# Performance work log

Measured on AMD Instinct MI355X. Metric: run time of the kernel, lower is better.

Reference implementation:

```python
import jax, jax.numpy as jnp
import numpy as np

B, N, DIM = 2, 512, 512
HEADS, DIM_HEAD, MAX_LEN = 8, 64, 1024


def _skew(QEr):
    # pad last dim on the left by 1, reshape (n, n+1) -> (n+1, n), drop first row
    padded = jnp.pad(QEr, ((0, 0), (0, 0), (0, 0), (1, 0)))
    b, h, r, c = padded.shape
    return padded.reshape(b, h, c, r)[:, :, 1:, :]


def _fft_multiply_parallel(A, x):
    # A: [b,h,n,n] decay matrix; x: [b,h,n,d]
    b, h, n, d = x.shape
    # y = [last column of A, first row of A] -> [b,h,2n]
    y = jnp.concatenate([A[:, :, :, -1], A[:, :, 0, :]], axis=-1)
    v = jnp.concatenate([x, jnp.zeros_like(x)], axis=-2)  # zero-pad rows n -> 2n
    # Faithful to the original torch code: fftn over ALL axes (incl. batch/head),
    # then ifft over the LAST axis only, then slice back to n rows.
    H = jnp.fft.fftn(y)[:, :, :, None] * jnp.fft.fftn(v)
    return jnp.fft.ifft(H)[:, :, :n, :]


def _forward(x, Wq, Wk, Wv, Er):
    b, n, _ = x.shape

    def split_heads(t):
        return t.reshape(b, n, HEADS, DIM_HEAD).transpose(0, 2, 1, 3)  # [b,h,n,d]

    q = split_heads(x @ Wq)
    k = split_heads(x @ Wk)
    v = split_heads(x @ Wv)
    # global (Frobenius) norm over the full tensor, as torch.norm(t)
    q = q / jnp.linalg.norm(q)
    k = k / jnp.linalg.norm(k)
    q_ = jax.nn.elu(q)
    k_ = jax.nn.elu(k)

    Er_t = Er[MAX_LEN - n:, :].T        # [d, n]
    QEr = q @ Er_t                       # [b,h,n,n]
    c = jnp.exp(_skew(QEr))              # relative-position decay, [b,h,n,n]

    a_1 = jnp.einsum('bhnx,bhny->bhnxy', k_, v).reshape(b, HEADS, n, DIM_HEAD * DIM_HEAD)
    d_2 = _fft_multiply_parallel(c, k_)                                   # [b,h,n,d] complex
    d_1 = _fft_multiply_parallel(c, a_1).reshape(b, HEADS, n, DIM_HEAD, DIM_HEAD)

    top = jnp.einsum('bhnx,bhnyz->bhnz', q_, d_1)    # complex [b,h,n,d]
    bottom = jnp.einsum('bhnx,bhny->bhny', q_, d_2)  # complex [b,h,n,d]
    return top / bottom


def setup_inputs() -> dict:
    key = jax.random.key(0)
    k1, k2, k3, k4, k5 = jax.random.split(key, 5)
    s = jnp.float32(1.0 / np.sqrt(DIM))
    return {
        'x': jax.random.normal(k1, (B, N, DIM), dtype=jnp.float32),
        'Wq': jax.random.normal(k2, (DIM, HEADS * DIM_HEAD), dtype=jnp.float32) * s,
        'Wk': jax.random.normal(k3, (DIM, HEADS * DIM_HEAD), dtype=jnp.float32) * s,
        'Wv': jax.random.normal(k4, (DIM, HEADS * DIM_HEAD), dtype=jnp.float32) * s,
        'Er': jax.random.normal(k5, (MAX_LEN, DIM_HEAD), dtype=jnp.float32),
    }


def reference(x, Wq, Wk, Wv, Er):
    return _forward(x, Wq, Wk, Wv, Er)
```

## Files before the change

### kernel.cpp

```cpp
#include <hip/hip_runtime.h>
#include <math.h>


#define DIMX 512
#define NPOS 512
#define PADIDX(m) ((m) + ((m) >> 4))

typedef unsigned short ushort_t;
typedef unsigned int uint_t;
typedef __bf16 bf16x8 __attribute__((ext_vector_type(8)));
typedef float floatx4 __attribute__((ext_vector_type(4)));

static __device__ inline ushort_t f2bf(float f) {
    uint_t u = __float_as_uint(f);
    u = u + 0x7FFFu + ((u >> 16) & 1u);
    return (ushort_t)(u >> 16);
}
static __device__ inline float bf2f(ushort_t h) {
    return __uint_as_float(((uint_t)h) << 16);
}

__global__ __launch_bounds__(256)
void conv_kernel(const float* __restrict__ x,
                 const float* __restrict__ Wk, const float* __restrict__ Wv,
                 ushort_t* __restrict__ xh, ushort_t* __restrict__ xl,
                 ushort_t* __restrict__ wth, ushort_t* __restrict__ wtl)
{
    const int blk = blockIdx.x;
    const int t = threadIdx.x;
    if (blk < 512) {
        const int idx4 = blk * 256 + t;
        const float4 v = ((const float4*)x)[idx4];
        const float vf[4] = {v.x, v.y, v.z, v.w};
        ushort_t h[4], l[4];
        #pragma unroll
        for (int e = 0; e < 4; ++e) {
            h[e] = f2bf(vf[e]);
            l[e] = f2bf(vf[e] - bf2f(h[e]));
        }
        ushort_t* ph = xh + (size_t)idx4 * 4;
        ushort_t* pl = xl + (size_t)idx4 * 4;
        #pragma unroll
        for (int e = 0; e < 4; ++e) { ph[e] = h[e]; pl[e] = l[e]; }
    } else {
        __shared__ float tile[32][33];
        const int b2 = blk - 512;
        const int s  = b2 >> 8;
        const int kt = (b2 >> 4) & 15;
        const int nt = b2 & 15;
        const int c  = t & 31, r4 = t >> 5;
        const float* __restrict__ W = s ? Wv : Wk;
        #pragma unroll
        for (int i = 0; i < 4; ++i) {
            const int row = r4 + i * 8;
            tile[row][c] = W[(size_t)(kt * 32 + row) * 512 + nt * 32 + c];
        }
        __syncthreads();
        #pragma unroll
        for (int i = 0; i < 4; ++i) {
            const int nl = r4 + i * 8;
            const float v = tile[c][nl];
            const ushort_t h = f2bf(v);
            const ushort_t l = f2bf(v - bf2f(h));
            const size_t o = (size_t)(s * 512 + nt * 32 + nl) * 512 + kt * 32 + c;
            wth[o] = h;
            wtl[o] = l;
        }
    }
}

__global__ __launch_bounds__(256)
void gemm_mfma_kernel(const ushort_t* __restrict__ xh, const ushort_t* __restrict__ xl,
                      const ushort_t* __restrict__ wth, const ushort_t* __restrict__ wtl,
                      float* __restrict__ K, float* __restrict__ V,
                      float* __restrict__ partials)
{
    const int blk = blockIdx.x;
    const int ct = blk >> 5;
    const int rt = blk & 31;
    const int t = threadIdx.x;
    const int w = t >> 6, lane = t & 63;
    const int qd = lane >> 4, lm = lane & 15;
    const int mrow  = rt * 32 + (w >> 1) * 16 + lm;
    const int ncol0 = ct * 64 + (w & 1) * 32;
    const size_t aoff  = (size_t)mrow * 512 + qd * 8;
    const size_t boff0 = (size_t)(ncol0 + lm) * 512 + qd * 8;
    const size_t boff1 = (size_t)(ncol0 + 16 + lm) * 512 + qd * 8;

    floatx4 acc0 = {0.f, 0.f, 0.f, 0.f};
    floatx4 acc1 = {0.f, 0.f, 0.f, 0.f};

    #pragma unroll
    for (int ks = 0; ks < 16; ++ks) {
        const int k0 = ks * 32;
        const bf16x8 Ah  = *(const bf16x8*)&xh [aoff  + k0];
        const bf16x8 Al  = *(const bf16x8*)&xl [aoff  + k0];
        const bf16x8 B0h = *(const bf16x8*)&wth[boff0 + k0];
        const bf16x8 B0l = *(const bf16x8*)&wtl[boff0 + k0];
        const bf16x8 B1h = *(const bf16x8*)&wth[boff1 + k0];
        const bf16x8 B1l = *(const bf16x8*)&wtl[boff1 + k0];
        acc0 = __builtin_amdgcn_mfma_f32_16x16x32_bf16(Ah, B0h, acc0, 0, 0, 0);
        acc0 = __builtin_amdgcn_mfma_f32_16x16x32_bf16(Ah, B0l, acc0, 0, 0, 0);
        acc0 = __builtin_amdgcn_mfma_f32_16x16x32_bf16(Al, B0h, acc0, 0, 0, 0);
        acc1 = __builtin_amdgcn_mfma_f32_16x16x32_bf16(Ah, B1h, acc1, 0, 0, 0);
        acc1 = __builtin_amdgcn_mfma_f32_16x16x32_bf16(Ah, B1l, acc1, 0, 0, 0);
        acc1 = __builtin_amdgcn_mfma_f32_16x16x32_bf16(Al, B1h, acc1, 0, 0, 0);
    }

    __shared__ float red[4];
    float ss = 0.f;
    const int orow0 = rt * 32 + (w >> 1) * 16 + qd * 4;
    float* __restrict__ O = (ct < 8) ? K : V;
    const int cb = (ct < 8) ? 0 : 512;
    const int c0 = ncol0 + lm - cb;
    #pragma unroll
    for (int r = 0; r < 4; ++r) {
        const size_t row = orow0 + r;
        const float v0 = acc0[r], v1 = acc1[r];
        O[row * 512 + c0]      = v0;
        O[row * 512 + c0 + 16] = v1;
        if (ct < 8) ss += v0 * v0 + v1 * v1;
    }
    #pragma unroll
    for (int off = 32; off > 0; off >>= 1)
        ss += __shfl_down(ss, off, 64);
    if (lane == 0) red[w] = ss;
    __syncthreads();
    if (t == 0) partials[blk] = red[0] + red[1] + red[2] + red[3];
}

__device__ __constant__ float C8[8] = {
    1.f, 0.70710678118654752440f, 0.f, -0.70710678118654752440f,
   -1.f, -0.70710678118654752440f, 0.f, 0.70710678118654752440f };
__device__ __constant__ float S8[8] = {
    0.f, -0.70710678118654752440f, -1.f, -0.70710678118654752440f,
    0.f,  0.70710678118654752440f,  1.f,  0.70710678118654752440f };

__global__ __launch_bounds__(256)
void stage1_kernel(const float* __restrict__ K,
                   const float* __restrict__ V,
                   const float* __restrict__ partials,
                   float2* __restrict__ Gk,
                   float2* __restrict__ Gp)
{
    const int m = blockIdx.x;
    const int t = threadIdx.x;
    __shared__ float kk[2][8][64];
    __shared__ float pp[2][8][64];
    __shared__ float skp[16][4];
    __shared__ float sk[2][8];
    __shared__ float sred[4];

    float p = partials[t] + partials[t + 256];
    #pragma unroll
    for (int off = 32; off > 0; off >>= 1)
        p += __shfl_down(p, off, 64);
    if ((t & 63) == 0) sred[t >> 6] = p;
    __syncthreads();
    const float scale = (float)(1.0 / sqrt((double)sred[0] + (double)sred[1] +
                                           (double)sred[2] + (double)sred[3]));

    {
        const int e0 = t * 4;
        const int b = e0 >> 9, rem = e0 & 511, h = rem >> 6, z = rem & 63;
        const size_t src = (size_t)(b * 512 + m) * DIMX + h * 64 + z;
        const float4 kv4 = *(const float4*)&K[src];
        const float4 vv4 = *(const float4*)&V[src];
        const float kf[4] = {kv4.x, kv4.y, kv4.z, kv4.w};
        const float vf[4] = {vv4.x, vv4.y, vv4.z, vv4.w};
        #pragma unroll
        for (int e = 0; e < 4; ++e) {
            const float kv = kf[e] * scale;
            kk[b][h][z + e] = kv > 0.f ? kv : expm1f(kv);
            pp[b][h][z + e] = vf[e];
        }
    }
    __syncthreads();
    if (t < 64) {
        const int bh = t >> 2, q = t & 3;
        float s = 0.f;
        #pragma unroll
        for (int zz = 0; zz < 16; ++zz) s += kk[bh >> 3][bh & 7][q * 16 + zz];
        skp[bh][q] = s;
    }
    __syncthreads();
    if (t < 16) sk[t >> 3][t & 7] = skp[t][0] + skp[t][1] + skp[t][2] + skp[t][3];
    __syncthreads();
    for (int e = t; e < 1024; e += 256) {
        const int b = e >> 9, rem = e & 511, h = rem >> 6, z = rem & 63;
        pp[b][h][z] *= sk[b][h];
    }
    __syncthreads();

    for (int e2 = t; e2 < 512; e2 += 256) {
        const int be = e2 >> 5;
        const int zp = e2 & 31;
        const int beta = be >> 3, eta = be & 7;
        float4 rk, rp;
        #pragma unroll
        for (int zz = 0; zz < 2; ++zz) {
            const int z = zp * 2 + zz;
            float gkr = 0.f, gki = 0.f, gpr = 0.f, gpi = 0.f;
            #pragma unroll
            for (int b = 0; b < 2; ++b) {
                const float sgn = (beta & b) ? -1.f : 1.f;
                #pragma unroll
                for (int h = 0; h < 8; ++h) {
                    const int ph = (eta * h) & 7;
                    const float cr = C8[ph], ci = S8[ph];
                    const float a = kk[b][h][z] * sgn;
                    gkr = fmaf(a, cr, gkr); gki = fmaf(a, ci, gki);
                    const float p2 = pp[b][h][z] * sgn;
                    gpr = fmaf(p2, cr, gpr); gpi = fmaf(p2, ci, gpi);
                }
            }
            if (zz == 0) { rk.x = gkr; rk.y = gki; rp.x = gpr; rp.y = gpi; }
            else         { rk.z = gkr; rk.w = gki; rp.z = gpr; rp.w = gpi; }
        }
        const size_t o = ((size_t)be * NPOS + m) * 64 + zp * 2;
        *(float4*)&Gk[o] = rk;
        *(float4*)&Gp[o] = rp;
    }
}

__global__ __launch_bounds__(256)
void fft_div_kernel(const float2* __restrict__ Gk,
                    const float2* __restrict__ Gp,
                    float* __restrict__ out, int out_cplx)
{
    const int blk = blockIdx.x;
    const int j  = blk & 7;
    const int l  = (blk >> 3) & 3;
    const int be = blk >> 5;
    const int zg = j * 4 + l;
    const int t  = threadIdx.x;

    __shared__ float2 g[4][1088];
    __shared__ float2 w[544];

    for (int jj = t; jj < 512; jj += 256) {
        double s, cc;
        sincos(-6.2831853071795864769 * (double)jj / 1024.0, &s, &cc);
        w[PADIDX(jj)] = make_float2((float)cc, (float)s);
    }
    __syncthreads();

    for (int e = t; e < 1024; e += 256) {
        const int a = e >> 9;
        const int m = e & 511;
        const float4 v4 = *(const float4*)&(a ? Gp : Gk)[((size_t)be * NPOS + m) * 64 + zg * 2];
        const float2 v0 = make_float2(v4.x, v4.y);
        const float2 v1 = make_float2(v4.z, v4.w);
        const float2 tw = w[PADIDX(m)];
        g[a * 2 + 0][PADIDX(m)] = v0;
        g[a * 2 + 1][PADIDX(m)] = v1;
        g[a * 2 + 0][PADIDX(m + 512)] = make_float2(v0.x * tw.x - v0.y * tw.y,
                                                    v0.x * tw.y + v0.y * tw.x);
        g[a * 2 + 1][PADIDX(m + 512)] = make_float2(v1.x * tw.x - v1.y * tw.y,
                                                    v1.x * tw.y + v1.y * tw.x);
    }
    __syncthreads();

    #pragma unroll
    for (int s = 1; s <= 9; ++s) {
        const int S = 512 >> s;
        const int lg = 9 - s;
        #pragma unroll
        for (int q = 0; q < 8; ++q) {
            const int B    = t + 256 * q;
            const int arr  = B >> 9;
            const int beta = B & 511;
            const int jb   = beta & (S - 1);
            const int seg  = beta >> lg;
            const int u    = (seg << (lg + 1)) + jb;
            const int v    = u + S;
            const float2 tw = w[PADIDX(jb << s)];
            const float2 A  = g[arr][PADIDX(u)];
            const float2 Bb = g[arr][PADIDX(v)];
            g[arr][PADIDX(u)] = make_float2(A.x + Bb.x, A.y + Bb.y);
            const float sr = A.x - Bb.x, si = A.y - Bb.y;
            g[arr][PADIDX(v)] = make_float2(sr * tw.x - si * tw.y,
                                            sr * tw.y + si * tw.x);
        }
        __syncthreads();
    }

    for (int e2 = t; e2 < 512; e2 += 256) {
        const int i  = e2;
        const int pi = PADIDX(2 * i);
        const int mu = (int)(__brev((unsigned)i) >> 23);
        float4 res;
        #pragma unroll
        for (int zi = 0; zi < 2; ++zi) {
            const float2 D  = g[zi][pi];
            const float2 Nm = g[2 + zi][pi];
            const float inv = 1.f / (D.x * D.x + D.y * D.y);
            const float rr = (Nm.x * D.x + Nm.y * D.y) * inv;
            const float ri = (Nm.y * D.x - Nm.x * D.y) * inv;
            if (zi == 0) { res.x = rr; res.y = ri; }
            else         { res.z = rr; res.w = ri; }
        }
        const size_t o = ((size_t)be * NPOS + mu) * 64 + zg * 2;
        if (out_cplx) {
            *(float4*)&((float2*)out)[o] = res;
        } else {
            out[o]     = res.x;
            out[o + 1] = res.z;
        }
    }
}

__global__ __launch_bounds__(256)
void gemm_kv_kernel(const float* __restrict__ x,
                    const float* __restrict__ Wk,
                    const float* __restrict__ Wv,
                    float* __restrict__ K,
                    float* __restrict__ V,
                    float* __restrict__ partials)
{
    const int blk  = blockIdx.x;
    const int sel  = (blk >> 2) & 1;
    const int cg2  = blk & 3;
    const int rt   = blk >> 3;
    const int row0 = rt * 16;
    const int col0 = cg2 * 128;
    const int t    = threadIdx.x;
    const int tc   = t & 31;
    const int tr   = t >> 5;
    const float* __restrict__ W   = sel ? Wv : Wk;
    float* __restrict__       Out = sel ? V  : K;

    __shared__ float xs[16][DIMX];
    __shared__ float red[4];

    #pragma unroll
    for (int j = 0; j < 8; ++j) {
        const int f = t + j * 256;
        const int row = f >> 7, c4 = f & 127;
        *(float4*)&xs[row][c4 * 4] = *(const float4*)&x[(size_t)(row0 + row) * DIMX + c4 * 4];
    }
    __syncthreads();

    const float* Wb = W + col0 + tc * 4;
    float4 wA[8], wB[8];
    #pragma unroll
    for (int j = 0; j < 8; ++j) wA[j] = *(const float4*)&Wb[(size_t)(j) * DIMX];
    #pragma unroll
    for (int j = 0; j < 8; ++j) wB[j] = *(const float4*)&Wb[(size_t)(8 + j) * DIMX];

    float acc[2][4] = {{0,0,0,0},{0,0,0,0}};
    const int r0 = tr * 2;

    #define COMPUTE_CHUNK(WREG, CH)                                            \
        {   float4 xv0a = *(const float4*)&xs[r0][(CH) * 8];                   \
            float4 xv0b = *(const float4*)&xs[r0][(CH) * 8 + 4];               \
            float4 xv1a = *(const float4*)&xs[r0 + 1][(CH) * 8];               \
            float4 xv1b = *(const float4*)&xs[r0 + 1][(CH) * 8 + 4];           \
            _Pragma("unroll")                                                  \
            for (int kk = 0; kk < 4; ++kk) {                                   \
                const float x0 = (&xv0a.x)[kk], x1 = (&xv1a.x)[kk];            \
                _Pragma("unroll")                                              \
                for (int cc = 0; cc < 4; ++cc) {                               \
                    acc[0][cc] = fmaf(x0, (&WREG[kk].x)[cc], acc[0][cc]);      \
                    acc[1][cc] = fmaf(x1, (&WREG[kk].x)[cc], acc[1][cc]);      \
                } }                                                            \
            _Pragma("unroll")                                                  \
            for (int kk = 0; kk < 4; ++kk) {                                   \
                const float x0 = (&xv0b.x)[kk], x1 = (&xv1b.x)[kk];            \
                _Pragma("unroll")                                              \
                for (int cc = 0; cc < 4; ++cc) {                               \
                    acc[0][cc] = fmaf(x0, (&WREG[kk + 4].x)[cc], acc[0][cc]);  \
                    acc[1][cc] = fmaf(x1, (&WREG[kk + 4].x)[cc], acc[1][cc]);  \
                } } }

    for (int ch = 0; ch < 64; ch += 2) {
        COMPUTE_CHUNK(wA, ch)
        if (ch < 62) {
            #pragma unroll
            for (int j = 0; j < 8; ++j)
                wA[j] = *(const float4*)&Wb[(size_t)((ch + 2) * 8 + j) * DIMX];
        }
        COMPUTE_CHUNK(wB, ch + 1)
        if (ch < 62) {
            #pragma unroll
            for (int j = 0; j < 8; ++j)
                wB[j] = *(const float4*)&Wb[(size_t)((ch + 3) * 8 + j) * DIMX];
        }
    }
    #undef COMPUTE_CHUNK

    float ss = 0.f;
    #pragma unroll
    for (int i = 0; i < 2; ++i) {
        const int row = row0 + r0 + i;
        const float4 o = make_float4(acc[i][0], acc[i][1], acc[i][2], acc[i][3]);
        *(float4*)&Out[(size_t)row * DIMX + col0 + tc * 4] = o;
        ss += o.x * o.x + o.y * o.y + o.z * o.z + o.w * o.w;
    }
    if (sel == 0) {
        #pragma unroll
        for (int off = 32; off > 0; off >>= 1)
            ss += __shfl_down(ss, off, 64);
        if ((t & 63) == 0) red[t >> 6] = ss;
        __syncthreads();
        if (t == 0) partials[blk] = red[0] + red[1] + red[2] + red[3];
    } else {
        if (t == 0) partials[blk] = 0.f;
    }
}

__global__ __launch_bounds__(256)
void mdft_fallback_kernel(const float2* __restrict__ Gk,
                          const float2* __restrict__ Gp,
                          float* __restrict__ out,
                          int out_cplx)
{
    const int blk = blockIdx.x;
    const int be = blk >> 6, z = blk & 63;
    const int t = threadIdx.x;
    __shared__ float2 gk[512];
    __shared__ float2 gp[512];
    __shared__ float2 w[1024];

    for (int m = t; m < 512; m += 256) {
        const size_t idx = ((size_t)be * NPOS + m) * 64 + z;
        gk[m] = Gk[idx];
        gp[m] = Gp[idx];
    }
    for (int jj = t; jj < 1024; jj += 256) {
        double s, c;
        sincos(-6.2831853071795864769 * (double)jj / 1024.0, &s, &c);
        w[jj] = make_float2((float)c, (float)s);
    }
    __syncthreads();

    #pragma unroll
    for (int half = 0; half < 2; ++half) {
        const int mu = t + half * 256;
        double dr = 0.0, di = 0.0, nr = 0.0, ni = 0.0;
        int idx = 0;
        for (int m = 0; m < 512; ++m) {
            const float2 tw = w[idx];
            idx = (idx + mu) & 1023;
            const float2 a = gk[m];
            dr += (double)(a.x * tw.x - a.y * tw.y);
            di += (double)(a.x * tw.y + a.y * tw.x);
            const float2 p = gp[m];
            nr += (double)(p.x * tw.x - p.y * tw.y);
            ni += (double)(p.x * tw.y + p.y * tw.x);
        }
        const double dmag = dr * dr + di * di;
        const double orr = (nr * dr + ni * di) / dmag;
        const double oii = (ni * dr - nr * di) / dmag;
        const size_t o = ((size_t)be * NPOS + mu) * 64 + z;
        if (out_cplx) {
            out[2 * o]     = (float)orr;
            out[2 * o + 1] = (float)oii;
        } else {
            out[o] = (float)orr;
        }
    }
}

extern "C" void kernel_launch(void* const* d_in, const int* in_sizes, int n_in,
                              void* d_out, int out_size, void* d_ws, size_t ws_size,
                              hipStream_t stream)
{
    const float* x  = (const float*)d_in[0];
    const float* Wk = (const float*)d_in[2];
    const float* Wv = (const float*)d_in[3];
    float* out = (float*)d_out;

    char* ws = (char*)d_ws;
    float*  K    = (float*)(ws);
    float*  V    = (float*)(ws + (size_t)2097152);
    float2* Gk   = (float2*)(ws + (size_t)4194304);
    float*  part = (float*)(ws + (size_t)8388608);
    const int out_cplx = (out_size >= 2 * 2 * 8 * 512 * 64) ? 1 : 0;

    const bool ws_big = (ws_size >= (size_t)20971520);
    float2* Gp = ws_big ? (float2*)(ws + (size_t)8390656)
                        : (float2*)d_out;

    if (ws_big) {
        ushort_t* xh  = (ushort_t*)(ws + (size_t)16777216);
        ushort_t* xl  = (ushort_t*)(ws + (size_t)17825792);
        ushort_t* wth = (ushort_t*)(ws + (size_t)18874368);
        ushort_t* wtl = (ushort_t*)(ws + (size_t)19922944);
        hipLaunchKernelGGL(conv_kernel, dim3(1024), dim3(256), 0, stream,
                           x, Wk, Wv, xh, xl, wth, wtl);
        hipLaunchKernelGGL(gemm_mfma_kernel, dim3(512), dim3(256), 0, stream,
                           xh, xl, wth, wtl, K, V, part);
        hipLaunchKernelGGL(stage1_kernel, dim3(512), dim3(256), 0, stream,
                           K, V, part, Gk, Gp);
        hipLaunchKernelGGL(fft_div_kernel, dim3(512), dim3(256), 0, stream,
                           Gk, Gp, out, out_cplx);
    } else {
        hipLaunchKernelGGL(gemm_kv_kernel, dim3(512), dim3(256), 0, stream,
                           x, Wk, Wv, K, V, part);
        hipLaunchKernelGGL(stage1_kernel, dim3(512), dim3(256), 0, stream,
                           K, V, part, Gk, Gp);
        hipLaunchKernelGGL(mdft_fallback_kernel, dim3(1024), dim3(256), 0, stream,
                           Gk, Gp, out, out_cplx);
    }
}
```

Baseline: 110.0 us.

## Register-blocked radix-8 FFT passes and precomputed twiddle table in fft_div_kernel

Replaces the nine shared-memory radix-2 FFT stages, each followed by a barrier, with three register-blocked passes of eight-point butterflies. Each wave handles one array, and the last pass only computes the even outputs that are consumed. Twiddle factors are now computed once with double-precision sincos in extra blocks of conv_kernel and stored in workspace, instead of being recomputed in every fft_div block. This reduces LDS traffic, barriers and per-block double-precision trig, at the cost of a global twiddle buffer and more complex indexing that has to match the previous butterfly order exactly.

Result: faster. 105.8 us (-3.8%).

```diff
diff --git a/kernel.cpp b/kernel.cpp
--- a/kernel.cpp
+++ b/kernel.cpp
@@ -20,11 +20,19 @@
     return __uint_as_float(((uint_t)h) << 16);
 }
 
+#define BFLY(lo, hi, tw) do {                                   \
+    const float sr_ = (lo).x - (hi).x, si_ = (lo).y - (hi).y;   \
+    (lo).x += (hi).x; (lo).y += (hi).y;                         \
+    (hi).x = sr_ * (tw).x - si_ * (tw).y;                       \
+    (hi).y = sr_ * (tw).y + si_ * (tw).x;                       \
+} while (0)
+
 __global__ __launch_bounds__(256)
 void conv_kernel(const float* __restrict__ x,
                  const float* __restrict__ Wk, const float* __restrict__ Wv,
                  ushort_t* __restrict__ xh, ushort_t* __restrict__ xl,
-                 ushort_t* __restrict__ wth, ushort_t* __restrict__ wtl)
+                 ushort_t* __restrict__ wth, ushort_t* __restrict__ wtl,
+                 float2* __restrict__ twd)
 {
     const int blk = blockIdx.x;
     const int t = threadIdx.x;
@@ -42,7 +50,7 @@
         ushort_t* pl = xl + (size_t)idx4 * 4;
         #pragma unroll
         for (int e = 0; e < 4; ++e) { ph[e] = h[e]; pl[e] = l[e]; }
-    } else {
+    } else if (blk < 1024) {
         __shared__ float tile[32][33];
         const int b2 = blk - 512;
         const int s  = b2 >> 8;
@@ -66,6 +74,11 @@
             wth[o] = h;
             wtl[o] = l;
         }
+    } else {
+        const int jj = (blk - 1024) * 256 + t;
+        double s, cc;
+        sincos(-6.2831853071795864769 * (double)jj / 1024.0, &s, &cc);
+        twd[jj] = make_float2((float)cc, (float)s);
     }
 }
 
@@ -226,6 +239,7 @@
 __global__ __launch_bounds__(256)
 void fft_div_kernel(const float2* __restrict__ Gk,
                     const float2* __restrict__ Gp,
+                    const float2* __restrict__ twd,
                     float* __restrict__ out, int out_cplx)
 {
     const int blk = blockIdx.x;
@@ -238,11 +252,8 @@
     __shared__ float2 g[4][1088];
     __shared__ float2 w[544];
 
-    for (int jj = t; jj < 512; jj += 256) {
-        double s, cc;
-        sincos(-6.2831853071795864769 * (double)jj / 1024.0, &s, &cc);
-        w[PADIDX(jj)] = make_float2((float)cc, (float)s);
-    }
+    for (int jj = t; jj < 512; jj += 256)
+        w[PADIDX(jj)] = twd[jj];
     __syncthreads();
 
     for (int e = t; e < 1024; e += 256) {
@@ -261,29 +272,101 @@
     }
     __syncthreads();
 
-    #pragma unroll
-    for (int s = 1; s <= 9; ++s) {
-        const int S = 512 >> s;
-        const int lg = 9 - s;
-        #pragma unroll
-        for (int q = 0; q < 8; ++q) {
-            const int B    = t + 256 * q;
-            const int arr  = B >> 9;
-            const int beta = B & 511;
-            const int jb   = beta & (S - 1);
-            const int seg  = beta >> lg;
-            const int u    = (seg << (lg + 1)) + jb;
-            const int v    = u + S;
-            const float2 tw = w[PADIDX(jb << s)];
-            const float2 A  = g[arr][PADIDX(u)];
-            const float2 Bb = g[arr][PADIDX(v)];
-            g[arr][PADIDX(u)] = make_float2(A.x + Bb.x, A.y + Bb.y);
-            const float sr = A.x - Bb.x, si = A.y - Bb.y;
-            g[arr][PADIDX(v)] = make_float2(sr * tw.x - si * tw.y,
-                                            sr * tw.y + si * tw.x);
-        }
-        __syncthreads();
-    }
+    const int wv   = t >> 6;
+    const int lane = t & 63;
+
+    #pragma unroll
+    for (int q = 0; q < 2; ++q) {
+        const int arr = wv;
+        const int h   = q;
+        const int jo  = lane;
+        float2 f[8];
+        #pragma unroll
+        for (int k = 0; k < 8; ++k)
+            f[k] = g[arr][PADIDX(h * 512 + jo + k * 64)];
+        #pragma unroll
+        for (int k = 0; k < 4; ++k) {
+            const float2 tw = w[PADIDX(2 * jo + 128 * k)];
+            BFLY(f[k], f[k + 4], tw);
+        }
+        {
+            const float2 tw0 = w[PADIDX(4 * jo)];
+            const float2 tw1 = w[PADIDX(4 * jo + 256)];
+            BFLY(f[0], f[2], tw0); BFLY(f[1], f[3], tw1);
+            BFLY(f[4], f[6], tw0); BFLY(f[5], f[7], tw1);
+        }
+        {
+            const float2 tw = w[PADIDX(8 * jo)];
+            BFLY(f[0], f[1], tw); BFLY(f[2], f[3], tw);
+            BFLY(f[4], f[5], tw); BFLY(f[6], f[7], tw);
+        }
+        #pragma unroll
+        for (int k = 0; k < 8; ++k)
+            g[arr][PADIDX(h * 512 + jo + k * 64)] = f[k];
+    }
+    __syncthreads();
+
+    #pragma unroll
+    for (int q = 0; q < 2; ++q) {
+        const int arr = wv;
+        const int b64 = q * 8 + (lane >> 3);
+        const int jo  = lane & 7;
+        const int e0  = b64 * 64 + jo;
+        float2 f[8];
+        #pragma unroll
+        for (int k = 0; k < 8; ++k)
+            f[k] = g[arr][PADIDX(e0 + 8 * k)];
+        #pragma unroll
+        for (int k = 0; k < 4; ++k) {
+            const float2 tw = w[PADIDX(16 * jo + 128 * k)];
+            BFLY(f[k], f[k + 4], tw);
+        }
+        {
+            const float2 tw0 = w[PADIDX(32 * jo)];
+            const float2 tw1 = w[PADIDX(32 * jo + 256)];
+            BFLY(f[0], f[2], tw0); BFLY(f[1], f[3], tw1);
+            BFLY(f[4], f[6], tw0); BFLY(f[5], f[7], tw1);
+        }
+        {
+            const float2 tw = w[PADIDX(64 * jo)];
+            BFLY(f[0], f[1], tw); BFLY(f[2], f[3], tw);
+            BFLY(f[4], f[5], tw); BFLY(f[6], f[7], tw);
+        }
+        #pragma unroll
+        for (int k = 0; k < 8; ++k)
+            g[arr][PADIDX(e0 + 8 * k)] = f[k];
+    }
+    __syncthreads();
+
+    #pragma unroll
+    for (int q = 0; q < 2; ++q) {
+        const int arr = wv;
+        const int b8  = q * 64 + lane;
+        const int e0  = b8 * 8;
+        float2 f[8];
+        #pragma unroll
+        for (int k = 0; k < 8; ++k)
+            f[k] = g[arr][PADIDX(e0 + k)];
+        BFLY(f[0], f[4], w[PADIDX(0)]);
+        BFLY(f[1], f[5], w[PADIDX(128)]);
+        BFLY(f[2], f[6], w[PADIDX(256)]);
+        BFLY(f[3], f[7], w[PADIDX(384)]);
+        {
+            const float2 tw0 = w[PADIDX(0)];
+            const float2 tw1 = w[PADIDX(256)];
+            BFLY(f[0], f[2], tw0); BFLY(f[1], f[3], tw1);
+            BFLY(f[4], f[6], tw0); BFLY(f[5], f[7], tw1);
+        }
+        f[0].x += f[1].x; f[0].y += f[1].y;
+        f[2].x += f[3].x; f[2].y += f[3].y;
+        f[4].x += f[5].x; f[4].y += f[5].y;
+        f[6].x += f[7].x; f[6].y += f[7].y;
+        g[arr][PADIDX(e0 + 0)] = f[0];
+        g[arr][PADIDX(e0 + 2)] = f[2];
+        g[arr][PADIDX(e0 + 4)] = f[4];
+        g[arr][PADIDX(e0 + 6)] = f[6];
+    }
+    __syncthreads();
 
     for (int e2 = t; e2 < 512; e2 += 256) {
         const int i  = e2;
@@ -487,14 +570,15 @@
         ushort_t* xl  = (ushort_t*)(ws + (size_t)17825792);
         ushort_t* wth = (ushort_t*)(ws + (size_t)18874368);
         ushort_t* wtl = (ushort_t*)(ws + (size_t)19922944);
-        hipLaunchKernelGGL(conv_kernel, dim3(1024), dim3(256), 0, stream,
-                           x, Wk, Wv, xh, xl, wth, wtl);
+        float2*   twd = (float2*)(ws + (size_t)12584960);
+        hipLaunchKernelGGL(conv_kernel, dim3(1026), dim3(256), 0, stream,
+                           x, Wk, Wv, xh, xl, wth, wtl, twd);
         hipLaunchKernelGGL(gemm_mfma_kernel, dim3(512), dim3(256), 0, stream,
                            xh, xl, wth, wtl, K, V, part);
         hipLaunchKernelGGL(stage1_kernel, dim3(512), dim3(256), 0, stream,
                            K, V, part, Gk, Gp);
         hipLaunchKernelGGL(fft_div_kernel, dim3(512), dim3(256), 0, stream,
-                           Gk, Gp, out, out_cplx);
+                           Gk, Gp, twd, out, out_cplx);
     } else {
         hipLaunchKernelGGL(gemm_kv_kernel, dim3(512), dim3(256), 0, stream,
                            x, Wk, Wv, K, V, part);
```
